# Performance work log

Measured on AMD Instinct MI355X. Metric: run time of the kernel, lower is better.

## Reference

```python
import jax, jax.numpy as jnp
import numpy as np

TEMPERATURE = 0.5
BATCH_SIZE = 4096
EPS = 1e-8  # torch.nn.CosineSimilarity default eps


def setup_inputs() -> dict:
    key = jax.random.key(0)
    k1, k2 = jax.random.split(key)
    z1 = jax.random.normal(k1, (BATCH_SIZE, 256), dtype=jnp.float32)
    z2 = jax.random.normal(k2, (BATCH_SIZE, 256), dtype=jnp.float32)
    return {"z1": z1, "z2": z2}


def reference(z1, z2):
    B = z1.shape[0]
    N = 2 * B
    reps = jnp.concatenate([z1, z2], axis=0)  # [N, D]
    # Cosine similarity (torch clamps each norm to eps before dividing)
    norms = jnp.maximum(jnp.linalg.norm(reps, axis=1, keepdims=True), EPS)
    z = reps / norms
    sim = z @ z.T  # [N, N] cosine similarity matrix

    # positives: diagonals at offsets +B and -B (they are identical by symmetry,
    # but keep the original concat order: [diag(+B), diag(-B)])
    l_pos = jnp.diagonal(sim, offset=B)
    r_pos = jnp.diagonal(sim, offset=-B)
    positives = jnp.concatenate([l_pos, r_pos])  # [N]

    inv_t = 1.0 / TEMPERATURE
    pos_logit = positives * inv_t  # logits[:, 0]

    # negatives are all off-diagonal entries of each row (the positive pair is
    # thus present twice in the logits, faithful to the original). CE with
    # label 0 => loss_i = logsumexp(logits_i) - logits_i[0].
    neg_logits = jnp.where(jnp.eye(N, dtype=bool), -jnp.inf, sim * inv_t)
    lse = jnp.logaddexp(pos_logit, jax.scipy.special.logsumexp(neg_logits, axis=1))
    loss = jnp.sum(lse - pos_logit) / N
    return loss
```

## Files before the change

### kernel.cpp

```cpp
#include <hip/hip_runtime.h>
#include <hip/hip_bf16.h>
#include <cstdint>
#include <cstddef>

#define BSZ   4096
#define NROW  8192
#define DIM   256
#define INV_T 2.0f
#define EPS_N 1e-8f

typedef __attribute__((ext_vector_type(8))) short bf16x8;
typedef __attribute__((ext_vector_type(4))) float f32x4;

__device__ __forceinline__ void load_lds16(const void* g, void* l) {
    __builtin_amdgcn_global_load_lds(
        (const __attribute__((address_space(1))) void*)g,
        (__attribute__((address_space(3))) void*)l,
        16, 0, 0);
}

__global__ void nt_normalize(const float* __restrict__ z1,
                             const float* __restrict__ z2,
                             __hip_bfloat16* __restrict__ zn) {
    const int row = blockIdx.x;
    const int tid = threadIdx.x;
    const float* src = (row < BSZ) ? (z1 + (size_t)row * DIM)
                                   : (z2 + (size_t)(row - BSZ) * DIM);
    float v = src[tid];
    float ss = v * v;
    #pragma unroll
    for (int off = 32; off; off >>= 1) ss += __shfl_xor(ss, off);
    __shared__ float red[4];
    __shared__ float rinv_s;
    if ((tid & 63) == 0) red[tid >> 6] = ss;
    __syncthreads();
    if (tid == 0) {
        float s = red[0] + red[1] + red[2] + red[3];
        rinv_s = 1.0f / fmaxf(sqrtf(s), EPS_N);
    }
    __syncthreads();
    zn[(size_t)row * DIM + tid] = __float2bfloat16(v * rinv_s);
}

__global__ __launch_bounds__(256)
void nt_gram(const __hip_bfloat16* __restrict__ zn,
             float* __restrict__ rowsum,
             float* __restrict__ pos) {
    const int bi = blockIdx.x, bj = blockIdx.y;
    if (bi > bj) return;

    __shared__ __hip_bfloat16 As[128 * 64];
    __shared__ __hip_bfloat16 Bs[128 * 64];

    const int t    = threadIdx.x;
    const int lane = t & 63;
    const int wave = t >> 6;
    const int wrow = (wave >> 1) * 64;
    const int wcol = (wave & 1) * 64;

    f32x4 acc[4][4] = {};

    const __hip_bfloat16* Ag = zn + (size_t)bi * 128 * DIM;
    const __hip_bfloat16* Bg = zn + (size_t)bj * 128 * DIM;

    const int srow  = t >> 3;
    const int schnk = t & 7;

    for (int k0 = 0; k0 < DIM; k0 += 64) {
        #pragma unroll
        for (int p = 0; p < 4; ++p) {
            const int row = p * 32 + srow;
            load_lds16(Ag + (size_t)row * DIM + k0 + schnk * 8,
                       (char*)As + p * 4096 + t * 16);
            load_lds16(Bg + (size_t)row * DIM + k0 + schnk * 8,
                       (char*)Bs + p * 4096 + t * 16);
        }
        __syncthreads();

        const int q   = lane >> 4;
        const int r16 = lane & 15;
        #pragma unroll
        for (int kk = 0; kk < 64; kk += 32) {
            bf16x8 af[4], bfr[4];
            #pragma unroll
            for (int mi = 0; mi < 4; ++mi) {
                const int m = wrow + mi * 16 + r16;
                af[mi] = *(const bf16x8*)((const char*)As + m * 128 + kk * 2 + q * 16);
            }
            #pragma unroll
            for (int ni = 0; ni < 4; ++ni) {
                const int n = wcol + ni * 16 + r16;
                bfr[ni] = *(const bf16x8*)((const char*)Bs + n * 128 + kk * 2 + q * 16);
            }
            #pragma unroll
            for (int mi = 0; mi < 4; ++mi)
                #pragma unroll
                for (int ni = 0; ni < 4; ++ni)
                    acc[mi][ni] = __builtin_amdgcn_mfma_f32_16x16x32_bf16(
                        af[mi], bfr[ni], acc[mi][ni], 0, 0, 0);
        }
        __syncthreads();
    }

    const int q = lane >> 4;
    const int c = lane & 15;
    const bool diag_block = (bi == bj);
    float colp[4] = {0.f, 0.f, 0.f, 0.f};

    #pragma unroll
    for (int mi = 0; mi < 4; ++mi) {
        #pragma unroll
        for (int r = 0; r < 4; ++r) {
            const int grow = bi * 128 + wrow + mi * 16 + q * 4 + r;
            float s = 0.f;
            #pragma unroll
            for (int ni = 0; ni < 4; ++ni) {
                const int gcol = bj * 128 + wcol + ni * 16 + c;
                const float val = acc[mi][ni][r];
                float e = __expf(val * INV_T);
                e = (grow == gcol) ? 0.f : e;
                s += e;
                colp[ni] += e;
                if (gcol == grow + BSZ) {
                    pos[grow] = val;
                    pos[gcol] = val;
                }
            }
            s += __shfl_xor(s, 1);
            s += __shfl_xor(s, 2);
            s += __shfl_xor(s, 4);
            s += __shfl_xor(s, 8);
            if (c == 0) atomicAdd(&rowsum[grow], s);
        }
    }
    if (!diag_block) {
        #pragma unroll
        for (int ni = 0; ni < 4; ++ni) {
            float cs = colp[ni];
            cs += __shfl_xor(cs, 16);
            cs += __shfl_xor(cs, 32);
            if (q == 0) atomicAdd(&rowsum[bj * 128 + wcol + ni * 16 + c], cs);
        }
    }
}

__global__ __launch_bounds__(256)
void nt_finalize(const float* __restrict__ rowsum,
                 const float* __restrict__ pos,
                 float* __restrict__ out) {
    const int i = blockIdx.x * 256 + threadIdx.x;
    const float pl  = pos[i] * INV_T;
    const float lse = logf(__expf(pl) + rowsum[i]);
    float v = (lse - pl) * (1.0f / NROW);
    #pragma unroll
    for (int off = 32; off; off >>= 1) v += __shfl_xor(v, off);
    __shared__ float red[4];
    if ((threadIdx.x & 63) == 0) red[threadIdx.x >> 6] = v;
    __syncthreads();
    if (threadIdx.x == 0)
        atomicAdd(out, red[0] + red[1] + red[2] + red[3]);
}

extern "C" void kernel_launch(void* const* d_in, const int* in_sizes, int n_in,
                              void* d_out, int out_size, void* d_ws, size_t ws_size,
                              hipStream_t stream) {
    const float* z1 = (const float*)d_in[0];
    const float* z2 = (const float*)d_in[1];
    float* out = (float*)d_out;

    __hip_bfloat16* zn = (__hip_bfloat16*)d_ws;
    float* rowsum = (float*)((char*)d_ws + (size_t)NROW * DIM * 2);
    float* pos    = rowsum + NROW;

    hipMemsetAsync(rowsum, 0, 2 * NROW * sizeof(float), stream);
    hipMemsetAsync(out, 0, sizeof(float), stream);

    nt_normalize<<<NROW, 256, 0, stream>>>(z1, z2, zn);
    dim3 grid(NROW / 128, NROW / 128);
    nt_gram<<<grid, 256, 0, stream>>>(zn, rowsum, pos);
    nt_finalize<<<NROW / 256, 256, 0, stream>>>(rowsum, pos, out);
}
```

Measured before the change: 115.3 us.

## Swizzle LDS tiles, compact triangular grid, drop memsets, vectorize normalize and finalize

Several changes land together. The gram kernel now launches only the 2080 upper-triangular tiles, decoding each linear block index into (bi, bj), so the 4096-block grid no longer spends half its blocks exiting early. It also XOR-swizzles the 16-byte chunks in LDS to avoid bank conflicts on the MFMA fragment reads. The normalize kernel handles one row per wave with float4 loads and needs no __syncthreads; it also zeroes rowsum, which replaces the two hipMemsetAsync calls. Finalize becomes a single 1024-thread block that writes out directly instead of using atomics, so out no longer has to be zeroed beforehand.

```diff
diff --git a/kernel.cpp b/kernel.cpp
--- a/kernel.cpp
+++ b/kernel.cpp
@@ -2,6 +2,7 @@
 #include <hip/hip_bf16.h>
 #include <cstdint>
 #include <cstddef>
+#include <math.h>
 
 #define BSZ   4096
 #define NROW  8192
@@ -12,6 +13,11 @@
 typedef __attribute__((ext_vector_type(8))) short bf16x8;
 typedef __attribute__((ext_vector_type(4))) float f32x4;
 
+__device__ __forceinline__ unsigned short f2bf(float x) {
+    __hip_bfloat16 h = __float2bfloat16(x);
+    return __builtin_bit_cast(unsigned short, h);
+}
+
 __device__ __forceinline__ void load_lds16(const void* g, void* l) {
     __builtin_amdgcn_global_load_lds(
         (const __attribute__((address_space(1))) void*)g,
@@ -19,35 +25,39 @@
         16, 0, 0);
 }
 
-__global__ void nt_normalize(const float* __restrict__ z1,
-                             const float* __restrict__ z2,
-                             __hip_bfloat16* __restrict__ zn) {
-    const int row = blockIdx.x;
-    const int tid = threadIdx.x;
+__global__ __launch_bounds__(256)
+void nt_normalize(const float* __restrict__ z1,
+                  const float* __restrict__ z2,
+                  __hip_bfloat16* __restrict__ zn,
+                  float* __restrict__ rowsum) {
+    const int wave = threadIdx.x >> 6;
+    const int lane = threadIdx.x & 63;
+    const int row  = blockIdx.x * 4 + wave;
     const float* src = (row < BSZ) ? (z1 + (size_t)row * DIM)
                                    : (z2 + (size_t)(row - BSZ) * DIM);
-    float v = src[tid];
-    float ss = v * v;
+    const float4 v = ((const float4*)src)[lane];
+    float ss = v.x * v.x + v.y * v.y + v.z * v.z + v.w * v.w;
     #pragma unroll
     for (int off = 32; off; off >>= 1) ss += __shfl_xor(ss, off);
-    __shared__ float red[4];
-    __shared__ float rinv_s;
-    if ((tid & 63) == 0) red[tid >> 6] = ss;
-    __syncthreads();
-    if (tid == 0) {
-        float s = red[0] + red[1] + red[2] + red[3];
-        rinv_s = 1.0f / fmaxf(sqrtf(s), EPS_N);
-    }
-    __syncthreads();
-    zn[(size_t)row * DIM + tid] = __float2bfloat16(v * rinv_s);
+    const float rinv = 1.0f / fmaxf(sqrtf(ss), EPS_N);
+    ushort4 o;
+    o.x = f2bf(v.x * rinv);
+    o.y = f2bf(v.y * rinv);
+    o.z = f2bf(v.z * rinv);
+    o.w = f2bf(v.w * rinv);
+    ((ushort4*)(zn + (size_t)row * DIM))[lane] = o;
+    if (lane == 0) rowsum[row] = 0.0f;
 }
 
 __global__ __launch_bounds__(256)
 void nt_gram(const __hip_bfloat16* __restrict__ zn,
              float* __restrict__ rowsum,
              float* __restrict__ pos) {
-    const int bi = blockIdx.x, bj = blockIdx.y;
-    if (bi > bj) return;
+    const int l = blockIdx.x;
+    int bi = (int)((129.0 - sqrt(16641.0 - 8.0 * (double)l)) * 0.5);
+    while (64 * (bi + 1) - (bi + 1) * bi / 2 <= l) ++bi;
+    while (64 * bi - bi * (bi - 1) / 2 > l) --bi;
+    const int bj = bi + (l - (64 * bi - bi * (bi - 1) / 2));
 
     __shared__ __hip_bfloat16 As[128 * 64];
     __shared__ __hip_bfloat16 Bs[128 * 64];
@@ -63,34 +73,38 @@
     const __hip_bfloat16* Ag = zn + (size_t)bi * 128 * DIM;
     const __hip_bfloat16* Bg = zn + (size_t)bj * 128 * DIM;
 
-    const int srow  = t >> 3;
-    const int schnk = t & 7;
+    const int srow = t >> 3;
+    const int sc   = (t & 7) ^ (srow & 7);
+
+    const int q   = lane >> 4;
+    const int r16 = lane & 15;
+    const int sw  = r16 & 7;
 
     for (int k0 = 0; k0 < DIM; k0 += 64) {
         #pragma unroll
         for (int p = 0; p < 4; ++p) {
             const int row = p * 32 + srow;
-            load_lds16(Ag + (size_t)row * DIM + k0 + schnk * 8,
+            load_lds16(Ag + (size_t)row * DIM + k0 + sc * 8,
                        (char*)As + p * 4096 + t * 16);
-            load_lds16(Bg + (size_t)row * DIM + k0 + schnk * 8,
+            load_lds16(Bg + (size_t)row * DIM + k0 + sc * 8,
                        (char*)Bs + p * 4096 + t * 16);
         }
         __syncthreads();
 
-        const int q   = lane >> 4;
-        const int r16 = lane & 15;
         #pragma unroll
         for (int kk = 0; kk < 64; kk += 32) {
+            const int cc = (kk >> 3) + q;
+            const int cpos = (cc ^ sw) << 4;
             bf16x8 af[4], bfr[4];
             #pragma unroll
             for (int mi = 0; mi < 4; ++mi) {
                 const int m = wrow + mi * 16 + r16;
-                af[mi] = *(const bf16x8*)((const char*)As + m * 128 + kk * 2 + q * 16);
+                af[mi] = *(const bf16x8*)((const char*)As + m * 128 + cpos);
             }
             #pragma unroll
             for (int ni = 0; ni < 4; ++ni) {
                 const int n = wcol + ni * 16 + r16;
-                bfr[ni] = *(const bf16x8*)((const char*)Bs + n * 128 + kk * 2 + q * 16);
+                bfr[ni] = *(const bf16x8*)((const char*)Bs + n * 128 + cpos);
             }
             #pragma unroll
             for (int mi = 0; mi < 4; ++mi)
@@ -102,7 +116,6 @@
         __syncthreads();
     }
 
-    const int q = lane >> 4;
     const int c = lane & 15;
     const bool diag_block = (bi == bj);
     float colp[4] = {0.f, 0.f, 0.f, 0.f};
@@ -144,21 +157,26 @@
     }
 }
 
-__global__ __launch_bounds__(256)
+__global__ __launch_bounds__(1024)
 void nt_finalize(const float* __restrict__ rowsum,
                  const float* __restrict__ pos,
                  float* __restrict__ out) {
-    const int i = blockIdx.x * 256 + threadIdx.x;
-    const float pl  = pos[i] * INV_T;
-    const float lse = logf(__expf(pl) + rowsum[i]);
-    float v = (lse - pl) * (1.0f / NROW);
+    float v = 0.f;
+    for (int i = threadIdx.x; i < NROW; i += 1024) {
+        const float pl = pos[i] * INV_T;
+        v += logf(__expf(pl) + rowsum[i]) - pl;
+    }
     #pragma unroll
     for (int off = 32; off; off >>= 1) v += __shfl_xor(v, off);
-    __shared__ float red[4];
+    __shared__ float red[16];
     if ((threadIdx.x & 63) == 0) red[threadIdx.x >> 6] = v;
     __syncthreads();
-    if (threadIdx.x == 0)
-        atomicAdd(out, red[0] + red[1] + red[2] + red[3]);
+    if (threadIdx.x == 0) {
+        float s = 0.f;
+        #pragma unroll
+        for (int w = 0; w < 16; ++w) s += red[w];
+        out[0] = s * (1.0f / NROW);
+    }
 }
 
 extern "C" void kernel_launch(void* const* d_in, const int* in_sizes, int n_in,
@@ -172,11 +190,7 @@
     float* rowsum = (float*)((char*)d_ws + (size_t)NROW * DIM * 2);
     float* pos    = rowsum + NROW;
 
-    hipMemsetAsync(rowsum, 0, 2 * NROW * sizeof(float), stream);
-    hipMemsetAsync(out, 0, sizeof(float), stream);
-
-    nt_normalize<<<NROW, 256, 0, stream>>>(z1, z2, zn);
-    dim3 grid(NROW / 128, NROW / 128);
-    nt_gram<<<grid, 256, 0, stream>>>(zn, rowsum, pos);
-    nt_finalize<<<NROW / 256, 256, 0, stream>>>(rowsum, pos, out);
+    nt_normalize<<<NROW / 4, 256, 0, stream>>>(z1, z2, zn, rowsum);
+    nt_gram<<<2080, 256, 0, stream>>>(zn, rowsum, pos);
+    nt_finalize<<<1, 1024, 0, stream>>>(rowsum, pos, out);
 }
```

After: 105.1 us. -8.8%, faster.
